# Performance work log

Measured on AMD Instinct MI355X. Metric: run time of the kernel, lower is better.

## Reference

```python
import jax, jax.numpy as jnp
import numpy as np

N_ACTIVE = 200000   # active voxels
GRID = 96           # spatial grid extent per axis
C = 128             # inplanes == outplanes
EPS = 1e-4          # scn BatchNormalization default eps


def _build_rulebook(n, g, seed=0):
    """Submanifold 3x3x3 rulebook: for each of 27 offsets, pairs (in_site, out_site)
    where coord[in] = coord[out] + offset and both sites are active. Padded to
    length n with dummy index n."""
    rng = np.random.default_rng(seed)
    lin = rng.choice(g ** 3, size=n, replace=False)
    coords = np.stack(np.unravel_index(lin, (g, g, g)), axis=1)  # [n,3]
    lut = -np.ones(g ** 3, dtype=np.int64)
    lut[lin] = np.arange(n)
    in_rows, out_rows = [], []
    for dx in (-1, 0, 1):
        for dy in (-1, 0, 1):
            for dz in (-1, 0, 1):
                nb = coords + np.array([dx, dy, dz])
                valid = np.all((nb >= 0) & (nb < g), axis=1)
                j = np.full(n, -1, dtype=np.int64)
                j[valid] = lut[np.ravel_multi_index(nb[valid].T, (g, g, g))]
                hit = j >= 0
                ii = j[hit]
                oi = np.nonzero(hit)[0].astype(np.int64)
                pad = n - ii.shape[0]
                in_rows.append(np.concatenate([ii, np.full(pad, n, dtype=np.int64)]))
                out_rows.append(np.concatenate([oi, np.full(pad, n, dtype=np.int64)]))
    return np.stack(in_rows), np.stack(out_rows)  # each [27, n]


def setup_inputs() -> dict:
    key = jax.random.key(0)
    k_feat, k_w1, k_w2 = jax.random.split(key, 3)
    in_idx_np, out_idx_np = _build_rulebook(N_ACTIVE, GRID)
    w_std = 1.0 / np.sqrt(27 * C)
    return {
        "features": jax.random.normal(k_feat, (N_ACTIVE, C), dtype=jnp.float32),
        "W1": jax.random.normal(k_w1, (27, C, C), dtype=jnp.float32) * w_std,
        "gamma1": jnp.ones((C,), jnp.float32),
        "beta1": jnp.zeros((C,), jnp.float32),
        "W2": jax.random.normal(k_w2, (27, C, C), dtype=jnp.float32) * w_std,
        "gamma2": jnp.ones((C,), jnp.float32),
        "beta2": jnp.zeros((C,), jnp.float32),
        "in_idx": jnp.asarray(in_idx_np),
        "out_idx": jnp.asarray(out_idx_np),
    }


def _subm_conv(feats, W, in_idx, out_idx):
    # feats: [N, Cin]; W: [27, Cin, Cout]; rulebook idx: [27, K] (dummy = N)
    n, c_in = feats.shape
    c_out = W.shape[-1]
    feats_pad = jnp.concatenate([feats, jnp.zeros((1, c_in), feats.dtype)], axis=0)

    def step(acc, t):
        ii, oi, w = t
        contrib = feats_pad[ii] @ w  # [K, Cout] gather -> GEMM
        return acc.at[oi].add(contrib), None  # scatter-add (dummy row n absorbs pad)

    acc0 = jnp.zeros((n + 1, c_out), feats.dtype)
    acc, _ = jax.lax.scan(step, acc0, (in_idx, out_idx, W))
    return acc[:n]


def _bn(x, gamma, beta):
    # batch-norm over active sites (training-mode batch stats)
    m = x.mean(axis=0)
    v = x.var(axis=0)
    return (x - m) * jax.lax.rsqrt(v + EPS) * gamma + beta


def reference(features, W1, gamma1, beta1, W2, gamma2, beta2, in_idx, out_idx):
    out = _subm_conv(features, W1, in_idx, out_idx)
    out = jax.nn.relu(_bn(out, gamma1, beta1))          # scn.BatchNormReLU
    out = _subm_conv(out, W2, in_idx, out_idx)
    out = _bn(out, gamma2, beta2)                       # scn.BatchNormalization
    return jax.nn.relu(out + features)                  # AddTable + ReLU
```

## Files before the change

kernel.cpp:

```cpp
#include <hip/hip_runtime.h>

#define NACT 200000
#define MPAD 200064
#define NBLK 1563
#define KOFF 27

typedef __bf16 bf16x8 __attribute__((ext_vector_type(8)));
typedef __bf16 bf16x4 __attribute__((ext_vector_type(4)));
typedef float f32x4 __attribute__((ext_vector_type(4)));

__device__ __forceinline__ void async_load16(const void* g, void* l) {
  __builtin_amdgcn_global_load_lds(
      (__attribute__((address_space(1))) void*)g,
      (__attribute__((address_space(3))) void*)l, 16, 0, 0);
}

__global__ void fill_g(int* __restrict__ G) {
  int i = blockIdx.x * 256 + threadIdx.x;
  if (i < KOFF * MPAD) G[i] = NACT;
}

__global__ void scatter_g(const int* __restrict__ ii, const int* __restrict__ oi,
                          int* __restrict__ G) {
  int i = blockIdx.x * 256 + threadIdx.x;
  if (i >= KOFF * NACT) return;
  int k = i / NACT;
  int o = oi[i];
  G[k * MPAD + o] = ii[i];
}

__global__ void fix_g(int* __restrict__ G) {
  int k = threadIdx.x;
  if (k < KOFF) G[k * MPAD + NACT] = NACT;
}

__global__ void cast_feats(const float* __restrict__ F, __bf16* __restrict__ X) {
  int i = blockIdx.x * 256 + threadIdx.x;
  if (i >= (NACT + 1) * 32) return;
  float4 v = (i < NACT * 32) ? ((const float4*)F)[i] : make_float4(0.f, 0.f, 0.f, 0.f);
  bf16x4 o = {(__bf16)v.x, (__bf16)v.y, (__bf16)v.z, (__bf16)v.w};
  *(bf16x4*)(X + (i << 2)) = o;
}

__global__ void prep_w(const float* __restrict__ W1, const float* __restrict__ W2,
                       __bf16* __restrict__ T1, __bf16* __restrict__ T2) {
  int i = blockIdx.x * 256 + threadIdx.x;
  if (i >= KOFF * 128 * 128) return;
  int k = i >> 14, rem = i & 16383, n = rem >> 7, c = rem & 127;
  int src = (k << 14) + (c << 7) + n;
  T1[i] = (__bf16)W1[src];
  T2[i] = (__bf16)W2[src];
}

__global__ __launch_bounds__(256, 4) void gemm_gather(
    const __bf16* __restrict__ X,
    const __bf16* __restrict__ WT,
    const int* __restrict__ G,
    __bf16* __restrict__ Y,
    float* __restrict__ Pst)
{
  __shared__ __bf16 Alds[128 * 64];
  __shared__ __bf16 Blds[128 * 64];
  const int t = threadIdx.x;
  const int lane = t & 63;
  const int w = t >> 6;
  const int wm = (w & 1) << 6;
  const int wn = (w >> 1) << 6;
  const int m_base = blockIdx.x << 7;
  const int r0 = t >> 3;
  const int scb = t & 7;
  const int l15 = lane & 15;
  const int q4 = lane >> 4;

  f32x4 acc[4][4];
#pragma unroll
  for (int i = 0; i < 4; ++i)
#pragma unroll
    for (int j = 0; j < 4; ++j) acc[i][j] = (f32x4){0.f, 0.f, 0.f, 0.f};

  for (int kk = 0; kk < KOFF; ++kk) {
    int rowA[4];
#pragma unroll
    for (int j = 0; j < 4; ++j)
      rowA[j] = G[kk * MPAD + m_base + r0 + j * 32];
    const __bf16* wb = WT + (kk << 14);
#pragma unroll
    for (int s = 0; s < 2; ++s) {
      const int c0 = s << 6;
      __syncthreads();
#pragma unroll
      for (int j = 0; j < 4; ++j) {
        const int r = r0 + j * 32;
        const int gcb = scb ^ (r & 7);
        async_load16(wb + (r << 7) + c0 + (gcb << 3), &Blds[(((r << 3) + scb) << 3)]);
        async_load16(X + (rowA[j] << 7) + c0 + (gcb << 3), &Alds[(((r << 3) + scb) << 3)]);
      }
      __syncthreads();
#pragma unroll
      for (int ks = 0; ks < 2; ++ks) {
        bf16x8 af[4], bfr[4];
        const int cb0 = (ks << 2) + q4;
#pragma unroll
        for (int mi = 0; mi < 4; ++mi) {
          const int r = wm + mi * 16 + l15;
          af[mi] = *(const bf16x8*)&Alds[(((r << 3) + (cb0 ^ (r & 7))) << 3)];
        }
#pragma unroll
        for (int ni = 0; ni < 4; ++ni) {
          const int r = wn + ni * 16 + l15;
          bfr[ni] = *(const bf16x8*)&Blds[(((r << 3) + (cb0 ^ (r & 7))) << 3)];
        }
#pragma unroll
        for (int mi = 0; mi < 4; ++mi)
#pragma unroll
          for (int ni = 0; ni < 4; ++ni)
            acc[mi][ni] = __builtin_amdgcn_mfma_f32_16x16x32_bf16(
                af[mi], bfr[ni], acc[mi][ni], 0, 0, 0);
      }
    }
  }

#pragma unroll
  for (int mi = 0; mi < 4; ++mi) {
#pragma unroll
    for (int ni = 0; ni < 4; ++ni) {
      const int col = wn + ni * 16 + l15;
#pragma unroll
      for (int rg = 0; rg < 4; ++rg) {
        const int row = m_base + wm + mi * 16 + (q4 << 2) + rg;
        Y[(row << 7) + col] = (__bf16)acc[mi][ni][rg];
      }
    }
  }

  float s[4], s2[4];
#pragma unroll
  for (int ni = 0; ni < 4; ++ni) {
    float a = 0.f, b = 0.f;
#pragma unroll
    for (int mi = 0; mi < 4; ++mi)
#pragma unroll
      for (int rg = 0; rg < 4; ++rg) {
        float v = acc[mi][ni][rg];
        a += v; b += v * v;
      }
    s[ni] = a; s2[ni] = b;
  }
#pragma unroll
  for (int ni = 0; ni < 4; ++ni) {
    s[ni]  += __shfl_xor(s[ni], 16);  s[ni]  += __shfl_xor(s[ni], 32);
    s2[ni] += __shfl_xor(s2[ni], 16); s2[ni] += __shfl_xor(s2[ni], 32);
  }
  float* sc = (float*)Alds;
  __syncthreads();
  if (q4 == 0) {
#pragma unroll
    for (int ni = 0; ni < 4; ++ni) {
      sc[(w << 6) + ni * 16 + l15]       = s[ni];
      sc[256 + (w << 6) + ni * 16 + l15] = s2[ni];
    }
  }
  __syncthreads();
  {
    const int kind = t >> 7, col = t & 127;
    const int w1 = (col >> 6) << 1;
    const float v = sc[kind * 256 + (w1 << 6) + (col & 63)] +
                    sc[kind * 256 + ((w1 + 1) << 6) + (col & 63)];
    Pst[(size_t)t * NBLK + blockIdx.x] = v;
  }
}

__global__ void stats_reduce(const float* __restrict__ P, float* __restrict__ st) {
  int b = blockIdx.x;
  const float* p = P + (size_t)b * NBLK;
  float s = 0.f;
  for (int i = threadIdx.x; i < NBLK; i += 256) s += p[i];
  for (int off = 32; off; off >>= 1) s += __shfl_down(s, off);
  __shared__ float ls[4];
  if ((threadIdx.x & 63) == 0) ls[threadIdx.x >> 6] = s;
  __syncthreads();
  if (threadIdx.x == 0) st[b] = ls[0] + ls[1] + ls[2] + ls[3];
}

__global__ void bn_coeffs(const float* __restrict__ st, const float* __restrict__ gamma,
                          const float* __restrict__ beta, float* __restrict__ co) {
  int c = threadIdx.x;
  float m = st[c] * (1.f / NACT);
  float v = st[128 + c] * (1.f / NACT) - m * m;
  float sc = gamma[c] * rsqrtf(v + 1e-4f);
  co[c] = sc;
  co[128 + c] = beta[c] - m * sc;
}

__global__ void bn_relu_cast(const __bf16* __restrict__ Y, const float* __restrict__ co,
                             __bf16* __restrict__ X2) {
  int i = blockIdx.x * 256 + threadIdx.x;
  if (i >= (NACT + 1) * 16) return;
  bf16x8 o;
  if (i < NACT * 16) {
    bf16x8 v = ((const bf16x8*)Y)[i];
    int cg = (i & 15) << 3;
#pragma unroll
    for (int e = 0; e < 8; ++e) {
      float x = fmaf((float)v[e], co[cg + e], co[128 + cg + e]);
      o[e] = (__bf16)fmaxf(x, 0.f);
    }
  } else {
#pragma unroll
    for (int e = 0; e < 8; ++e) o[e] = (__bf16)0.f;
  }
  ((bf16x8*)X2)[i] = o;
}

__global__ void bn_add_relu(const __bf16* __restrict__ Y, const float* __restrict__ co,
                            const float* __restrict__ F, float* __restrict__ O) {
  int i = blockIdx.x * 256 + threadIdx.x;
  if (i >= NACT * 16) return;
  bf16x8 v = ((const bf16x8*)Y)[i];
  float4 f0 = ((const float4*)F)[2 * i];
  float4 f1 = ((const float4*)F)[2 * i + 1];
  int cg = (i & 15) << 3;
  float4 o0, o1;
  o0.x = fmaxf(fmaf((float)v[0], co[cg + 0], co[128 + cg + 0]) + f0.x, 0.f);
  o0.y = fmaxf(fmaf((float)v[1], co[cg + 1], co[128 + cg + 1]) + f0.y, 0.f);
  o0.z = fmaxf(fmaf((float)v[2], co[cg + 2], co[128 + cg + 2]) + f0.z, 0.f);
  o0.w = fmaxf(fmaf((float)v[3], co[cg + 3], co[128 + cg + 3]) + f0.w, 0.f);
  o1.x = fmaxf(fmaf((float)v[4], co[cg + 4], co[128 + cg + 4]) + f1.x, 0.f);
  o1.y = fmaxf(fmaf((float)v[5], co[cg + 5], co[128 + cg + 5]) + f1.y, 0.f);
  o1.z = fmaxf(fmaf((float)v[6], co[cg + 6], co[128 + cg + 6]) + f1.z, 0.f);
  o1.w = fmaxf(fmaf((float)v[7], co[cg + 7], co[128 + cg + 7]) + f1.w, 0.f);
  ((float4*)O)[2 * i] = o0;
  ((float4*)O)[2 * i + 1] = o1;
}

extern "C" void kernel_launch(void* const* d_in, const int* in_sizes, int n_in,
                              void* d_out, int out_size, void* d_ws, size_t ws_size,
                              hipStream_t stream) {
  const float* features = (const float*)d_in[0];
  const float* W1       = (const float*)d_in[1];
  const float* gamma1   = (const float*)d_in[2];
  const float* beta1    = (const float*)d_in[3];
  const float* W2       = (const float*)d_in[4];
  const float* gamma2   = (const float*)d_in[5];
  const float* beta2    = (const float*)d_in[6];
  const int* in_idx     = (const int*)d_in[7];
  const int* out_idx    = (const int*)d_in[8];

  char* ws = (char*)d_ws;
  size_t off = 0;
  int*    G   = (int*)(ws + off);    off += (size_t)KOFF * MPAD * 4;
  __bf16* X   = (__bf16*)(ws + off); off += (size_t)(NACT + 1) * 128 * 2;
  __bf16* T1  = (__bf16*)(ws + off); off += (size_t)KOFF * 128 * 128 * 2;
  __bf16* T2  = (__bf16*)(ws + off); off += (size_t)KOFF * 128 * 128 * 2;
  __bf16* Y   = (__bf16*)(ws + off); off += (size_t)MPAD * 128 * 2;
  float*  Pst = (float*)(ws + off);  off += (size_t)256 * NBLK * 4;
  float*  st  = (float*)(ws + off);  off += 4096;

  fill_g<<<(KOFF * MPAD + 255) / 256, 256, 0, stream>>>(G);
  scatter_g<<<(KOFF * NACT + 255) / 256, 256, 0, stream>>>(in_idx, out_idx, G);
  fix_g<<<1, 32, 0, stream>>>(G);
  cast_feats<<<((NACT + 1) * 32 + 255) / 256, 256, 0, stream>>>(features, X);
  prep_w<<<(KOFF * 128 * 128 + 255) / 256, 256, 0, stream>>>(W1, W2, T1, T2);

  gemm_gather<<<NBLK, 256, 0, stream>>>(X, T1, G, Y, Pst);
  stats_reduce<<<256, 256, 0, stream>>>(Pst, st);
  bn_coeffs<<<1, 128, 0, stream>>>(st, gamma1, beta1, st + 512);
  bn_relu_cast<<<((NACT + 1) * 16 + 255) / 256, 256, 0, stream>>>(Y, st + 512, X);

  gemm_gather<<<NBLK, 256, 0, stream>>>(X, T2, G, Y, Pst);
  stats_reduce<<<256, 256, 0, stream>>>(Pst, st);
  bn_coeffs<<<1, 128, 0, stream>>>(st, gamma2, beta2, st + 768);
  bn_add_relu<<<(NACT * 16 + 255) / 256, 256, 0, stream>>>(Y, st + 768, features, (float*)d_out);
}
```

Baseline: 609.9 us.

## Load weights directly to registers, fuse prep kernels, merge stats and coeffs

The gather-GEMM no longer stages the weight tile in LDS. It reads weights straight from global memory into registers, using a pre-permuted layout so each lane's bf16x8 fragment is contiguous, and launch bounds drop from 4 to 3 blocks per CU. The separate fill/scatter/cast/weight-prep kernels become one memset plus one multi-role kernel that clamps invalid gather indices, and the stats reduction is fused with the BN coefficient computation. The aim is to cut LDS traffic, barriers and launch overhead, at the cost of more global/L2 weight reads per block and possibly lower occupancy.

```diff
diff --git a/kernel.cpp b/kernel.cpp
--- a/kernel.cpp
+++ b/kernel.cpp
@@ -5,6 +5,10 @@
 #define NBLK 1563
 #define KOFF 27
 
+#define SCAT_B 21094
+#define CAST_B 25001
+#define PREPW_B 1728
+
 typedef __bf16 bf16x8 __attribute__((ext_vector_type(8)));
 typedef __bf16 bf16x4 __attribute__((ext_vector_type(4)));
 typedef float f32x4 __attribute__((ext_vector_type(4)));
@@ -15,52 +19,42 @@
       (__attribute__((address_space(3))) void*)l, 16, 0, 0);
 }
 
-__global__ void fill_g(int* __restrict__ G) {
-  int i = blockIdx.x * 256 + threadIdx.x;
-  if (i < KOFF * MPAD) G[i] = NACT;
-}
-
-__global__ void scatter_g(const int* __restrict__ ii, const int* __restrict__ oi,
-                          int* __restrict__ G) {
-  int i = blockIdx.x * 256 + threadIdx.x;
-  if (i >= KOFF * NACT) return;
-  int k = i / NACT;
-  int o = oi[i];
-  G[k * MPAD + o] = ii[i];
-}
-
-__global__ void fix_g(int* __restrict__ G) {
-  int k = threadIdx.x;
-  if (k < KOFF) G[k * MPAD + NACT] = NACT;
-}
-
-__global__ void cast_feats(const float* __restrict__ F, __bf16* __restrict__ X) {
-  int i = blockIdx.x * 256 + threadIdx.x;
-  if (i >= (NACT + 1) * 32) return;
-  float4 v = (i < NACT * 32) ? ((const float4*)F)[i] : make_float4(0.f, 0.f, 0.f, 0.f);
-  bf16x4 o = {(__bf16)v.x, (__bf16)v.y, (__bf16)v.z, (__bf16)v.w};
-  *(bf16x4*)(X + (i << 2)) = o;
-}
-
-__global__ void prep_w(const float* __restrict__ W1, const float* __restrict__ W2,
-                       __bf16* __restrict__ T1, __bf16* __restrict__ T2) {
-  int i = blockIdx.x * 256 + threadIdx.x;
-  if (i >= KOFF * 128 * 128) return;
-  int k = i >> 14, rem = i & 16383, n = rem >> 7, c = rem & 127;
-  int src = (k << 14) + (c << 7) + n;
-  T1[i] = (__bf16)W1[src];
-  T2[i] = (__bf16)W2[src];
-}
-
-__global__ __launch_bounds__(256, 4) void gemm_gather(
+__global__ void prep_all(const int* __restrict__ ii, const int* __restrict__ oi,
+                         int* __restrict__ G,
+                         const float* __restrict__ F, __bf16* __restrict__ X,
+                         const float* __restrict__ W1, const float* __restrict__ W2,
+                         __bf16* __restrict__ T1, __bf16* __restrict__ T2) {
+  int b = blockIdx.x;
+  if (b < SCAT_B) {
+    int i = b * 256 + threadIdx.x;
+    if (i < KOFF * NACT) {
+      int o = oi[i];
+      if (o < NACT) G[(i / NACT) * MPAD + o] = ii[i];
+    }
+  } else if (b < SCAT_B + CAST_B) {
+    int i = (b - SCAT_B) * 256 + threadIdx.x;
+    if (i < (NACT + 1) * 32) {
+      float4 v = (i < NACT * 32) ? ((const float4*)F)[i] : make_float4(0.f, 0.f, 0.f, 0.f);
+      bf16x4 o = {(__bf16)v.x, (__bf16)v.y, (__bf16)v.z, (__bf16)v.w};
+      *(bf16x4*)(X + (i << 2)) = o;
+    }
+  } else {
+    int i = (b - SCAT_B - CAST_B) * 256 + threadIdx.x;
+    int kk = i >> 14, r = i & 16383, cc = r >> 10, n = (r >> 3) & 127, e = r & 7;
+    int src = (kk << 14) + ((cc << 3) + e) * 128 + n;
+    T1[i] = (__bf16)W1[src];
+    T2[i] = (__bf16)W2[src];
+  }
+}
+
+__global__ __launch_bounds__(256, 3) void gemm_gather(
     const __bf16* __restrict__ X,
-    const __bf16* __restrict__ WT,
+    const __bf16* __restrict__ B2,
     const int* __restrict__ G,
     __bf16* __restrict__ Y,
     float* __restrict__ Pst)
 {
   __shared__ __bf16 Alds[128 * 64];
-  __shared__ __bf16 Blds[128 * 64];
   const int t = threadIdx.x;
   const int lane = t & 63;
   const int w = t >> 6;
@@ -81,9 +75,10 @@
   for (int kk = 0; kk < KOFF; ++kk) {
     int rowA[4];
 #pragma unroll
-    for (int j = 0; j < 4; ++j)
-      rowA[j] = G[kk * MPAD + m_base + r0 + j * 32];
-    const __bf16* wb = WT + (kk << 14);
+    for (int j = 0; j < 4; ++j) {
+      int g = G[kk * MPAD + m_base + r0 + j * 32];
+      rowA[j] = g < NACT ? g : NACT;
+    }
 #pragma unroll
     for (int s = 0; s < 2; ++s) {
       const int c0 = s << 6;
@@ -92,30 +87,45 @@
       for (int j = 0; j < 4; ++j) {
         const int r = r0 + j * 32;
         const int gcb = scb ^ (r & 7);
-        async_load16(wb + (r << 7) + c0 + (gcb << 3), &Blds[(((r << 3) + scb) << 3)]);
         async_load16(X + (rowA[j] << 7) + c0 + (gcb << 3), &Alds[(((r << 3) + scb) << 3)]);
       }
+      const __bf16* bbase = B2 + (((kk << 4) + (s << 3) + q4) << 10) + ((wn + l15) << 3);
+      bf16x8 b0[4], b1[4];
+#pragma unroll
+      for (int ni = 0; ni < 4; ++ni)
+        b0[ni] = *(const bf16x8*)(bbase + (ni << 7));
       __syncthreads();
 #pragma unroll
-      for (int ks = 0; ks < 2; ++ks) {
-        bf16x8 af[4], bfr[4];
-        const int cb0 = (ks << 2) + q4;
+      for (int ni = 0; ni < 4; ++ni)
+        b1[ni] = *(const bf16x8*)(bbase + (1 << 12) + (ni << 7));
+      {
+        bf16x8 af[4];
+#pragma unroll
+        for (int mi = 0; mi < 4; ++mi) {
+          const int r = wm + mi * 16 + l15;
+          af[mi] = *(const bf16x8*)&Alds[(((r << 3) + (q4 ^ (r & 7))) << 3)];
+        }
+#pragma unroll
+        for (int mi = 0; mi < 4; ++mi)
+#pragma unroll
+          for (int ni = 0; ni < 4; ++ni)
+            acc[mi][ni] = __builtin_amdgcn_mfma_f32_16x16x32_bf16(
+                af[mi], b0[ni], acc[mi][ni], 0, 0, 0);
+      }
+      {
+        bf16x8 af[4];
+        const int cb0 = 4 + q4;
 #pragma unroll
         for (int mi = 0; mi < 4; ++mi) {
           const int r = wm + mi * 16 + l15;
           af[mi] = *(const bf16x8*)&Alds[(((r << 3) + (cb0 ^ (r & 7))) << 3)];
         }
 #pragma unroll
-        for (int ni = 0; ni < 4; ++ni) {
-          const int r = wn + ni * 16 + l15;
-          bfr[ni] = *(const bf16x8*)&Blds[(((r << 3) + (cb0 ^ (r & 7))) << 3)];
-        }
-#pragma unroll
         for (int mi = 0; mi < 4; ++mi)
 #pragma unroll
           for (int ni = 0; ni < 4; ++ni)
             acc[mi][ni] = __builtin_amdgcn_mfma_f32_16x16x32_bf16(
-                af[mi], bfr[ni], acc[mi][ni], 0, 0, 0);
+                af[mi], b1[ni], acc[mi][ni], 0, 0, 0);
       }
     }
   }
@@ -170,26 +180,33 @@
   }
 }
 
-__global__ void stats_reduce(const float* __restrict__ P, float* __restrict__ st) {
-  int b = blockIdx.x;
-  const float* p = P + (size_t)b * NBLK;
-  float s = 0.f;
-  for (int i = threadIdx.x; i < NBLK; i += 256) s += p[i];
-  for (int off = 32; off; off >>= 1) s += __shfl_down(s, off);
-  __shared__ float ls[4];
-  if ((threadIdx.x & 63) == 0) ls[threadIdx.x >> 6] = s;
+__global__ void stats_coeffs(const float* __restrict__ P, const float* __restrict__ gamma,
+                             const float* __restrict__ beta, float* __restrict__ co) {
+  int c = blockIdx.x;
+  float s = 0.f, s2 = 0.f;
+  for (int i = threadIdx.x; i < NBLK; i += 256) {
+    s  += P[(size_t)c * NBLK + i];
+    s2 += P[(size_t)(128 + c) * NBLK + i];
+  }
+  for (int off = 32; off; off >>= 1) {
+    s  += __shfl_down(s, off);
+    s2 += __shfl_down(s2, off);
+  }
+  __shared__ float ls[8];
+  if ((threadIdx.x & 63) == 0) {
+    ls[threadIdx.x >> 6]     = s;
+    ls[4 + (threadIdx.x >> 6)] = s2;
+  }
   __syncthreads();
-  if (threadIdx.x == 0) st[b] = ls[0] + ls[1] + ls[2] + ls[3];
-}
-
-__global__ void bn_coeffs(const float* __restrict__ st, const float* __restrict__ gamma,
-                          const float* __restrict__ beta, float* __restrict__ co) {
-  int c = threadIdx.x;
-  float m = st[c] * (1.f / NACT);
-  float v = st[128 + c] * (1.f / NACT) - m * m;
-  float sc = gamma[c] * rsqrtf(v + 1e-4f);
-  co[c] = sc;
-  co[128 + c] = beta[c] - m * sc;
+  if (threadIdx.x == 0) {
+    float S  = ls[0] + ls[1] + ls[2] + ls[3];
+    float S2 = ls[4] + ls[5] + ls[6] + ls[7];
+    float m = S * (1.f / NACT);
+    float v = S2 * (1.f / NACT) - m * m;
+    float scale = gamma[c] * rsqrtf(v + 1e-4f);
+    co[c] = scale;
+    co[128 + c] = beta[c] - m * scale;
+  }
 }
 
 __global__ void bn_relu_cast(const __bf16* __restrict__ Y, const float* __restrict__ co,
@@ -256,19 +273,16 @@
   float*  Pst = (float*)(ws + off);  off += (size_t)256 * NBLK * 4;
   float*  st  = (float*)(ws + off);  off += 4096;
 
-  fill_g<<<(KOFF * MPAD + 255) / 256, 256, 0, stream>>>(G);
-  scatter_g<<<(KOFF * NACT + 255) / 256, 256, 0, stream>>>(in_idx, out_idx, G);
-  fix_g<<<1, 32, 0, stream>>>(G);
-  cast_feats<<<((NACT + 1) * 32 + 255) / 256, 256, 0, stream>>>(features, X);
-  prep_w<<<(KOFF * 128 * 128 + 255) / 256, 256, 0, stream>>>(W1, W2, T1, T2);
+  hipMemsetAsync(G, 0x7F, (size_t)KOFF * MPAD * 4, stream);
+
+  prep_all<<<SCAT_B + CAST_B + PREPW_B, 256, 0, stream>>>(
+      in_idx, out_idx, G, features, X, W1, W2, T1, T2);
 
   gemm_gather<<<NBLK, 256, 0, stream>>>(X, T1, G, Y, Pst);
-  stats_reduce<<<256, 256, 0, stream>>>(Pst, st);
-  bn_coeffs<<<1, 128, 0, stream>>>(st, gamma1, beta1, st + 512);
-  bn_relu_cast<<<((NACT + 1) * 16 + 255) / 256, 256, 0, stream>>>(Y, st + 512, X);
+  stats_coeffs<<<128, 256, 0, stream>>>(Pst, gamma1, beta1, st);
+  bn_relu_cast<<<((NACT + 1) * 16 + 255) / 256, 256, 0, stream>>>(Y, st, X);
 
   gemm_gather<<<NBLK, 256, 0, stream>>>(X, T2, G, Y, Pst);
-  stats_reduce<<<256, 256, 0, stream>>>(Pst, st);
-  bn_coeffs<<<1, 128, 0, stream>>>(st, gamma2, beta2, st + 768);
-  bn_add_relu<<<(NACT * 16 + 255) / 256, 256, 0, stream>>>(Y, st + 768, features, (float*)d_out);
-}
+  stats_coeffs<<<128, 256, 0, stream>>>(Pst, gamma2, beta2, st + 256);
+  bn_add_relu<<<(NACT * 16 + 255) / 256, 256, 0, stream>>>(Y, st + 256, features, (float*)d_out);
+}
```

New measurement: 683.8 us. +12.1%, slower.
